# Performance work log

Measured on AMD Instinct MI355X. Metric: run time of the kernel, lower is better.

The kernel has to match this reference:

```python
import jax, jax.numpy as jnp
import numpy as np

DIM = 1024
HEAD_DIM = 64
NUM_HEADS = DIM // HEAD_DIM
SCALE = HEAD_DIM ** -0.5


def setup_inputs() -> dict:
    key = jax.random.key(0)
    ks = jax.random.split(key, 12)
    b, n = 4, 2048
    std = DIM ** -0.5
    inp = {
        'words': jax.random.normal(ks[0], (b, n, DIM), jnp.float32),
        'position': jax.random.normal(ks[1], (b, n, DIM), jnp.float32),
        'conscious': jax.random.normal(ks[2], (b, n, DIM), jnp.float32),
        # projection weights stored as [in, out] (torch Linear W^T)
        'w_wq': jax.random.normal(ks[3], (DIM, DIM), jnp.float32) * std,
        'w_wk': jax.random.normal(ks[4], (DIM, DIM), jnp.float32) * std,
        'w_wv': jax.random.normal(ks[5], (DIM, DIM), jnp.float32) * std,
        'w_pq': jax.random.normal(ks[6], (DIM, DIM), jnp.float32) * std,
        'w_pk': jax.random.normal(ks[7], (DIM, DIM), jnp.float32) * std,
        'w_cq': jax.random.normal(ks[8], (DIM, DIM), jnp.float32) * std,
        'w_ck': jax.random.normal(ks[9], (DIM, DIM), jnp.float32) * std,
        'w_out': jax.random.normal(ks[10], (DIM, DIM), jnp.float32) * std,
        'b_out': jax.random.normal(ks[11], (DIM,), jnp.float32) * 0.01,
    }
    return inp


def _heads(x):
    b, n, _ = x.shape
    return x.reshape(b, n, NUM_HEADS, HEAD_DIM).transpose(0, 2, 1, 3)  # b h n d


def reference(words, position, conscious, w_wq, w_wk, w_wv, w_pq, w_pk, w_cq, w_ck, w_out, b_out):
    # fused multi-source q/k: sum of three projections per source
    q = _heads(words @ w_wq + position @ w_pq + conscious @ w_cq)
    k = _heads(words @ w_wk + position @ w_pk + conscious @ w_ck)
    v = _heads(words @ w_wv)
    sim = jnp.einsum('bhid,bhjd->bhij', q, k) * SCALE
    attn = jax.nn.softmax(sim, axis=-1)
    out = jnp.einsum('bhij,bhjd->bhid', attn, v)
    b, h, n, d = out.shape
    out = out.transpose(0, 2, 1, 3).reshape(b, n, h * d)
    return out @ w_out + b_out
```

## Files before the change

kernel.cpp:

```cpp
#include <hip/hip_runtime.h>
#include <hip/hip_bf16.h>

typedef __bf16 bf16_t;
typedef __attribute__((ext_vector_type(8))) __bf16 bf16x8;
typedef __attribute__((ext_vector_type(4))) float f32x4;
typedef __attribute__((ext_vector_type(16))) float f32x16;

__device__ __forceinline__ void gld_lds16(const void* g, void* l) {
  __builtin_amdgcn_global_load_lds((const __attribute__((address_space(1))) void*)g,
                                   (__attribute__((address_space(3))) void*)l, 16, 0, 0);
}

__global__ __launch_bounds__(256) void cast_concat(
    const float* __restrict__ w, const float* __restrict__ p,
    const float* __restrict__ c, bf16_t* __restrict__ X)
{
  unsigned idx = blockIdx.x * 256u + threadIdx.x;
  unsigned src = idx >> 21;
  unsigned rem = idx & ((1u << 21) - 1);
  unsigned row = rem >> 8;
  unsigned k4  = (rem & 255u) * 4u;
  const float* s = (src == 0) ? w : (src == 1) ? p : c;
  f32x4 v = *(const f32x4*)(s + (size_t)row * 1024 + k4);
  ushort4 u;
  u.x = __builtin_bit_cast(unsigned short, (bf16_t)v[0]);
  u.y = __builtin_bit_cast(unsigned short, (bf16_t)v[1]);
  u.z = __builtin_bit_cast(unsigned short, (bf16_t)v[2]);
  u.w = __builtin_bit_cast(unsigned short, (bf16_t)v[3]);
  *(ushort4*)(X + (size_t)row * 3072 + src * 1024 + k4) = u;
}

__global__ __launch_bounds__(256) void transpose_all(
    const float* __restrict__ w_wq, const float* __restrict__ w_pq,
    const float* __restrict__ w_cq, const float* __restrict__ w_wk,
    const float* __restrict__ w_pk, const float* __restrict__ w_ck,
    const float* __restrict__ w_wv, const float* __restrict__ w_out,
    bf16_t* __restrict__ Wqkt, bf16_t* __restrict__ Wvt, bf16_t* __restrict__ Wot)
{
  __shared__ float t[32][33];
  const int z = blockIdx.z;
  const float* src; bf16_t* dst; int dstride, koff, roff;
  switch (z) {
    case 0: src = w_wq;  dst = Wqkt; dstride = 3072; koff = 0;    roff = 0;    break;
    case 1: src = w_pq;  dst = Wqkt; dstride = 3072; koff = 1024; roff = 0;    break;
    case 2: src = w_cq;  dst = Wqkt; dstride = 3072; koff = 2048; roff = 0;    break;
    case 3: src = w_wk;  dst = Wqkt; dstride = 3072; koff = 0;    roff = 1024; break;
    case 4: src = w_pk;  dst = Wqkt; dstride = 3072; koff = 1024; roff = 1024; break;
    case 5: src = w_ck;  dst = Wqkt; dstride = 3072; koff = 2048; roff = 1024; break;
    case 6: src = w_wv;  dst = Wvt;  dstride = 1024; koff = 0;    roff = 0;    break;
    default: src = w_out; dst = Wot; dstride = 1024; koff = 0;    roff = 0;    break;
  }
  int bx = blockIdx.x, by = blockIdx.y;
  int x = bx * 32 + threadIdx.x;
  int y0 = by * 32;
  for (int i = threadIdx.y; i < 32; i += 8)
    t[i][threadIdx.x] = src[(size_t)(y0 + i) * 1024 + x];
  __syncthreads();
  int n0 = bx * 32;
  for (int i = threadIdx.y; i < 32; i += 8)
    dst[(size_t)(n0 + i + roff) * dstride + koff + y0 + threadIdx.x] =
        (bf16_t)t[threadIdx.x][i];
}

__global__ __launch_bounds__(512, 2) void gemm256_qk(
    const bf16_t* __restrict__ A, int lda,
    const bf16_t* __restrict__ Bt, int K,
    bf16_t* __restrict__ Qo, bf16_t* __restrict__ Ko, float scale, int nbx)
{
  __shared__ bf16_t As[2][256 * 64];
  __shared__ bf16_t Bs[2][256 * 64];

  const int tid = threadIdx.x;
  const int wave = tid >> 6, lane = tid & 63;
  const int wm = wave >> 2, wn = wave & 3;
  const int lrow = lane & 15, lch = lane >> 4;

  const int nwg = gridDim.x, cpx = nwg >> 3;
  const int id  = blockIdx.x;
  const int swz = (id & 7) * cpx + (id >> 3);
  const int mb = swz / nbx, nb = swz % nbx;
  const int m0 = mb * 256, n0 = nb * 256;

  const int srow = tid >> 3, spp = tid & 7;

  auto STAGE = [&](int buf, int k0) {
#pragma unroll
    for (int i = 0; i < 4; ++i) {
      int r = i * 64 + srow;
      int gsw = (spp ^ (r & 7)) * 8;
      gld_lds16(A + (size_t)(m0 + r) * lda + k0 + gsw, &As[buf][r * 64 + spp * 8]);
    }
#pragma unroll
    for (int i = 0; i < 4; ++i) {
      int r = i * 64 + srow;
      int gsw = (spp ^ (r & 7)) * 8;
      gld_lds16(Bt + (size_t)(n0 + r) * K + k0 + gsw, &Bs[buf][r * 64 + spp * 8]);
    }
  };

  const int NT = K >> 6;
  STAGE(0, 0);
  STAGE(1, 64);

  f32x4 acc[8][4] = {};

  for (int kt = 0; kt < NT; ++kt) {
    const int cur = kt & 1;
    if (kt < NT - 1) {
      asm volatile("s_waitcnt vmcnt(8)" ::: "memory");
    } else {
      asm volatile("s_waitcnt vmcnt(0)" ::: "memory");
    }
    asm volatile("s_barrier" ::: "memory");

#pragma unroll
    for (int ks = 0; ks < 2; ++ks) {
      bf16x8 af[8], bfr[4];
#pragma unroll
      for (int m = 0; m < 8; ++m) {
        int r = wm * 128 + m * 16 + lrow;
        af[m] = *(const bf16x8*)&As[cur][r * 64 + (((ks * 4 + lch) ^ (r & 7)) * 8)];
      }
#pragma unroll
      for (int n = 0; n < 4; ++n) {
        int r = wn * 64 + n * 16 + lrow;
        bfr[n] = *(const bf16x8*)&Bs[cur][r * 64 + (((ks * 4 + lch) ^ (r & 7)) * 8)];
      }
      __builtin_amdgcn_s_setprio(1);
#pragma unroll
      for (int m = 0; m < 8; ++m)
#pragma unroll
        for (int n = 0; n < 4; ++n)
          acc[m][n] = __builtin_amdgcn_mfma_f32_16x16x32_bf16(af[m], bfr[n], acc[m][n], 0, 0, 0);
      __builtin_amdgcn_s_setprio(0);
    }

    asm volatile("s_waitcnt lgkmcnt(0)" ::: "memory");
    asm volatile("s_barrier" ::: "memory");
    if (kt + 2 < NT) STAGE(cur, (kt + 2) * 64);
  }

  const int g = lane >> 4, cl = lane & 15;
#pragma unroll
  for (int m = 0; m < 8; ++m) {
    int m_base = m0 + wm * 128 + m * 16 + g * 4;
    int bb = m_base >> 11, nn = m_base & 2047;
#pragma unroll
    for (int n = 0; n < 4; ++n) {
      int col = n0 + wn * 64 + n * 16 + cl;
      bf16_t* dst = (col < 1024) ? Qo : Ko;
      int cc2 = col & 1023;
      float sc = (col < 1024) ? scale : 1.0f;
      int h = cc2 >> 6, d = cc2 & 63;
      size_t base = ((size_t)(bb * 16 + h) * 2048 + nn) * 64 + d;
#pragma unroll
      for (int r = 0; r < 4; ++r)
        dst[base + (size_t)r * 64] = (bf16_t)(acc[m][n][r] * sc);
    }
  }
}

template<int EPI>
__global__ __launch_bounds__(512, 2) void gemm128x256(
    const bf16_t* __restrict__ A, int lda,
    const bf16_t* __restrict__ Bt, int K,
    void* __restrict__ Cout, const float* __restrict__ bias)
{
  __shared__ bf16_t As[2][128 * 64];
  __shared__ bf16_t Bs[2][256 * 64];

  const int tid = threadIdx.x;
  const int wave = tid >> 6, lane = tid & 63;
  const int wm = wave >> 2, wn = wave & 3;
  const int lrow = lane & 15, lch = lane >> 4;

  const int nwg = gridDim.x, cpx = nwg >> 3;
  const int id  = blockIdx.x;
  const int swz = (id & 7) * cpx + (id >> 3);
  const int mb = swz >> 2, nb = swz & 3;
  const int m0 = mb * 128, n0 = nb * 256;

  const int srow = tid >> 3, spp = tid & 7;

  auto STAGE = [&](int buf, int k0) {
#pragma unroll
    for (int i = 0; i < 2; ++i) {
      int r = i * 64 + srow;
      int gsw = (spp ^ (r & 7)) * 8;
      gld_lds16(A + (size_t)(m0 + r) * lda + k0 + gsw, &As[buf][r * 64 + spp * 8]);
    }
#pragma unroll
    for (int i = 0; i < 4; ++i) {
      int r = i * 64 + srow;
      int gsw = (spp ^ (r & 7)) * 8;
      gld_lds16(Bt + (size_t)(n0 + r) * K + k0 + gsw, &Bs[buf][r * 64 + spp * 8]);
    }
  };

  const int NT = K >> 6;
  STAGE(0, 0);
  STAGE(1, 64);

  f32x4 acc[4][4] = {};

  for (int kt = 0; kt < NT; ++kt) {
    const int cur = kt & 1;
    if (kt < NT - 1) {
      asm volatile("s_waitcnt vmcnt(6)" ::: "memory");
    } else {
      asm volatile("s_waitcnt vmcnt(0)" ::: "memory");
    }
    asm volatile("s_barrier" ::: "memory");

#pragma unroll
    for (int ks = 0; ks < 2; ++ks) {
      bf16x8 af[4], bfr[4];
#pragma unroll
      for (int m = 0; m < 4; ++m) {
        int r = wm * 64 + m * 16 + lrow;
        af[m] = *(const bf16x8*)&As[cur][r * 64 + (((ks * 4 + lch) ^ (r & 7)) * 8)];
      }
#pragma unroll
      for (int n = 0; n < 4; ++n) {
        int r = wn * 64 + n * 16 + lrow;
        bfr[n] = *(const bf16x8*)&Bs[cur][r * 64 + (((ks * 4 + lch) ^ (r & 7)) * 8)];
      }
      __builtin_amdgcn_s_setprio(1);
#pragma unroll
      for (int m = 0; m < 4; ++m)
#pragma unroll
        for (int n = 0; n < 4; ++n)
          acc[m][n] = __builtin_amdgcn_mfma_f32_16x16x32_bf16(af[m], bfr[n], acc[m][n], 0, 0, 0);
      __builtin_amdgcn_s_setprio(0);
    }

    asm volatile("s_waitcnt lgkmcnt(0)" ::: "memory");
    asm volatile("s_barrier" ::: "memory");
    if (kt + 2 < NT) STAGE(cur, (kt + 2) * 64);
  }

  const int g = lane >> 4, cl = lane & 15;
  if (EPI == 1) {
    bf16_t* Vo = (bf16_t*)Cout;
#pragma unroll
    for (int m = 0; m < 4; ++m) {
      int m_base = m0 + wm * 64 + m * 16 + g * 4;
      int bb = m_base >> 11, nn = m_base & 2047;
#pragma unroll
      for (int n = 0; n < 4; ++n) {
        int col = n0 + wn * 64 + n * 16 + cl;
        int h = col >> 6, d = col & 63;
        ushort4 u;
        u.x = __builtin_bit_cast(unsigned short, (bf16_t)acc[m][n][0]);
        u.y = __builtin_bit_cast(unsigned short, (bf16_t)acc[m][n][1]);
        u.z = __builtin_bit_cast(unsigned short, (bf16_t)acc[m][n][2]);
        u.w = __builtin_bit_cast(unsigned short, (bf16_t)acc[m][n][3]);
        *(ushort4*)(Vo + ((size_t)(bb * 16 + h) * 64 + d) * 2048 + nn) = u;
      }
    }
  } else {
    float* Co = (float*)Cout;
#pragma unroll
    for (int m = 0; m < 4; ++m) {
      int m_base = m0 + wm * 64 + m * 16 + g * 4;
#pragma unroll
      for (int n = 0; n < 4; ++n) {
        int col = n0 + wn * 64 + n * 16 + cl;
        float bv = bias[col];
#pragma unroll
        for (int r = 0; r < 4; ++r)
          Co[(size_t)(m_base + r) * 1024 + col] = acc[m][n][r] + bv;
      }
    }
  }
}

__global__ __launch_bounds__(512, 2) void attn_kernel(
    const bf16_t* __restrict__ Q, const bf16_t* __restrict__ Kb,
    const bf16_t* __restrict__ Vt, bf16_t* __restrict__ O)
{
  __shared__ bf16_t Ks[2][64 * 64];
  __shared__ bf16_t Vs[2][64 * 64];

  const int fid = blockIdx.x;
  const int swz = (fid & 7) * 64 + (fid >> 3);
  const int bh = swz >> 3, qt = swz & 7;
  const int bb = bh >> 4, h = bh & 15;

  const int tid = threadIdx.x, wave = tid >> 6, lane = tid & 63;
  const int lq = lane & 31;
  const int lh = lane >> 5;

  const bf16_t* Qb    = Q  + ((size_t)bh * 2048 + qt * 256) * 64;
  const bf16_t* Kbase = Kb + (size_t)bh * 2048 * 64;
  const bf16_t* Vbase = Vt + (size_t)bh * 64 * 2048;

  const int srow = tid >> 3, spp = tid & 7;
  const int sgr = (spp ^ (srow & 7)) * 8;

  auto STAGE_K = [&](int buf, int tile) {
    gld_lds16(Kbase + (size_t)(tile * 64 + srow) * 64 + sgr, &Ks[buf][tid * 8]);
  };
  auto STAGE_V = [&](int buf, int tile) {
    gld_lds16(Vbase + (size_t)srow * 2048 + tile * 64 + sgr, &Vs[buf][tid * 8]);
  };

  STAGE_K(0, 0); STAGE_V(0, 0); STAGE_K(1, 1);

  bf16x8 qf[4];
#pragma unroll
  for (int kf = 0; kf < 4; ++kf)
    qf[kf] = *(const bf16x8*)(Qb + (size_t)(wave * 32 + lq) * 64 + kf * 16 + lh * 8);

  f32x16 acc[2] = {};
  float m_run = -1.0e30f, l_run = 0.f;
  bf16x8 pb[4];

  auto QKT = [&](int tile, f32x16 (&st)[2]) {
    const int kb = tile & 1;
#pragma unroll
    for (int nb2 = 0; nb2 < 2; ++nb2) {
      int r = nb2 * 32 + lq;
      f32x16 z = {};
#pragma unroll
      for (int kf = 0; kf < 4; ++kf) {
        bf16x8 ka = *(const bf16x8*)&Ks[kb][r * 64 + (((kf * 2 + lh) ^ (r & 7)) * 8)];
        z = __builtin_amdgcn_mfma_f32_32x32x16_bf16(ka, qf[kf], z, 0, 0, 0);
      }
      st[nb2] = z;
    }
  };

  auto PV = [&](int tile) {
    const int vb = tile & 1;
#pragma unroll
    for (int ks = 0; ks < 4; ++ks)
#pragma unroll
      for (int db = 0; db < 2; ++db) {
        int r = db * 32 + lq;
        bf16x8 va = *(const bf16x8*)&Vs[vb][r * 64 + (((ks * 2 + lh) ^ (r & 7)) * 8)];
        acc[db] = __builtin_amdgcn_mfma_f32_32x32x16_bf16(va, pb[ks], acc[db], 0, 0, 0);
      }
  };

  auto SOFTMAX = [&](f32x16 (&st)[2]) {
    float tmax = fmaxf(st[0][0], st[0][1]);
#pragma unroll
    for (int nb2 = 0; nb2 < 2; ++nb2)
#pragma unroll
      for (int rg = (nb2 ? 0 : 2); rg < 16; rg += 2)
        tmax = fmaxf(fmaxf(tmax, st[nb2][rg]), st[nb2][rg + 1]);
    tmax = fmaxf(tmax, __shfl_xor(tmax, 32));

    if (!__all(tmax <= m_run + 8.0f)) {
      float mnew = fmaxf(m_run, tmax);
      float corr = __builtin_amdgcn_exp2f(m_run - mnew);
      m_run = mnew;
      l_run *= corr;
#pragma unroll
      for (int db = 0; db < 2; ++db)
#pragma unroll
        for (int rg = 0; rg < 16; ++rg)
          acc[db][rg] *= corr;
    }

    float sm = 0.f;
#pragma unroll
    for (int nb2 = 0; nb2 < 2; ++nb2)
#pragma unroll
      for (int rg = 0; rg < 16; ++rg) {
        float p = __builtin_amdgcn_exp2f(st[nb2][rg] - m_run);
        st[nb2][rg] = p;
        sm += p;
      }
    sm += __shfl_xor(sm, 32);
    l_run += sm;

#pragma unroll
    for (int ks = 0; ks < 4; ++ks) {
      const int nb2 = ks >> 1;
      const int R = (ks & 1) * 8;
      unsigned x0, x1, y0, y1;
      asm("v_cvt_pk_bf16_f32 %0, %1, %2" : "=v"(x0) : "v"(st[nb2][R + 0]), "v"(st[nb2][R + 1]));
      asm("v_cvt_pk_bf16_f32 %0, %1, %2" : "=v"(x1) : "v"(st[nb2][R + 2]), "v"(st[nb2][R + 3]));
      asm("v_cvt_pk_bf16_f32 %0, %1, %2" : "=v"(y0) : "v"(st[nb2][R + 4]), "v"(st[nb2][R + 5]));
      asm("v_cvt_pk_bf16_f32 %0, %1, %2" : "=v"(y1) : "v"(st[nb2][R + 6]), "v"(st[nb2][R + 7]));
      asm volatile("v_permlane32_swap_b32 %0, %1" : "+v"(x0), "+v"(y0));
      asm volatile("v_permlane32_swap_b32 %0, %1" : "+v"(x1), "+v"(y1));
      int4 pw;
      pw.x = (int)x0; pw.y = (int)x1; pw.z = (int)y0; pw.w = (int)y1;
      pb[ks] = __builtin_bit_cast(bf16x8, pw);
    }
  };

  asm volatile("s_waitcnt vmcnt(0)" ::: "memory");
  __builtin_amdgcn_s_barrier();
  asm volatile("" ::: "memory");
  {
    f32x16 st[2];
    QKT(0, st);
    SOFTMAX(st);
  }
  asm volatile("s_waitcnt lgkmcnt(0)" ::: "memory");
  __builtin_amdgcn_s_barrier();
  asm volatile("" ::: "memory");

  for (int t = 0; t < 32; ++t) {
    if (t < 30)       { STAGE_V((t + 1) & 1, t + 1); STAGE_K(t & 1, t + 2); }
    else if (t == 30) { STAGE_V(1, 31); }
    if (t < 30)       asm volatile("s_waitcnt vmcnt(2)" ::: "memory");
    else if (t == 30) asm volatile("s_waitcnt vmcnt(1)" ::: "memory");
    else              asm volatile("s_waitcnt vmcnt(0)" ::: "memory");
    __builtin_amdgcn_s_barrier();
    asm volatile("" ::: "memory");

    f32x16 st[2];
    __builtin_amdgcn_s_setprio(1);
    if (t < 31) QKT(t + 1, st);
    PV(t);
    __builtin_amdgcn_s_setprio(0);
    if (t < 31) SOFTMAX(st);

    asm volatile("s_waitcnt lgkmcnt(0)" ::: "memory");
    __builtin_amdgcn_s_barrier();
    asm volatile("" ::: "memory");
  }

  float inv = 1.0f / l_run;
  int nn = qt * 256 + wave * 32 + lq;
  size_t obase = ((size_t)bb * 2048 + nn) * 1024 + h * 64;
#pragma unroll
  for (int db = 0; db < 2; ++db)
#pragma unroll
    for (int rr = 0; rr < 4; ++rr) {
      ushort4 u;
      u.x = __builtin_bit_cast(unsigned short, (bf16_t)(acc[db][rr * 4 + 0] * inv));
      u.y = __builtin_bit_cast(unsigned short, (bf16_t)(acc[db][rr * 4 + 1] * inv));
      u.z = __builtin_bit_cast(unsigned short, (bf16_t)(acc[db][rr * 4 + 2] * inv));
      u.w = __builtin_bit_cast(unsigned short, (bf16_t)(acc[db][rr * 4 + 3] * inv));
      *(ushort4*)(O + obase + db * 32 + rr * 8 + lh * 4) = u;
    }
}

extern "C" void kernel_launch(void* const* d_in, const int* in_sizes, int n_in,
                              void* d_out, int out_size, void* d_ws, size_t ws_size,
                              hipStream_t stream) {
  const float* words     = (const float*)d_in[0];
  const float* position  = (const float*)d_in[1];
  const float* conscious = (const float*)d_in[2];
  const float* w_wq  = (const float*)d_in[3];
  const float* w_wk  = (const float*)d_in[4];
  const float* w_wv  = (const float*)d_in[5];
  const float* w_pq  = (const float*)d_in[6];
  const float* w_pk  = (const float*)d_in[7];
  const float* w_cq  = (const float*)d_in[8];
  const float* w_ck  = (const float*)d_in[9];
  const float* w_out = (const float*)d_in[10];
  const float* b_out = (const float*)d_in[11];

  char* ws = (char*)d_ws;
  bf16_t* Xcat = (bf16_t*)(ws);
  bf16_t* Wqkt = (bf16_t*)(ws + 50331648);
  bf16_t* Wvt  = (bf16_t*)(ws + 62914560);
  bf16_t* Wot  = (bf16_t*)(ws + 65011712);
  bf16_t* Qb   = (bf16_t*)(ws + 67108864);
  bf16_t* Kbf  = (bf16_t*)(ws + 83886080);
  bf16_t* Vtb  = (bf16_t*)(ws + 100663296);
  bf16_t* Ob   = (bf16_t*)(ws + 117440512);

  cast_concat<<<24576, 256, 0, stream>>>(words, position, conscious, Xcat);

  transpose_all<<<dim3(32, 32, 8), dim3(32, 8), 0, stream>>>(
      w_wq, w_pq, w_cq, w_wk, w_pk, w_ck, w_wv, w_out, Wqkt, Wvt, Wot);

  gemm256_qk<<<256, 512, 0, stream>>>(Xcat, 3072, Wqkt, 3072, Qb, Kbf,
                                      0.125f * 1.44269504f, 8);
  gemm128x256<1><<<256, 512, 0, stream>>>(Xcat, 3072, Wvt, 1024, Vtb, nullptr);

  attn_kernel<<<512, 512, 0, stream>>>(Qb, Kbf, Vtb, Ob);

  gemm128x256<2><<<256, 512, 0, stream>>>(Ob, 1024, Wot, 1024, (float*)d_out, b_out);
}
```

Baseline: 288.6 us.

## Process two 32-row query blocks per wave in attention, halving block threads

The attention kernel now uses 256 threads (4 waves) per block, and each wave handles 64 query rows as two 32-row sub-blocks. Each K/V fragment read from LDS feeds two MFMAs, which halves LDS read traffic per MFMA. Staging is split so each thread issues two async loads per tile, and the vmcnt waits are adjusted to match. The cost is roughly double the accumulator and score registers per wave, fewer waves per block to hide latency, and two softmax passes per wave.

```diff
diff --git a/kernel.cpp b/kernel.cpp
--- a/kernel.cpp
+++ b/kernel.cpp
@@ -275,7 +275,7 @@
   }
 }
 
-__global__ __launch_bounds__(512, 2) void attn_kernel(
+__global__ __launch_bounds__(256, 2) void attn_kernel(
     const bf16_t* __restrict__ Q, const bf16_t* __restrict__ Kb,
     const bf16_t* __restrict__ Vt, bf16_t* __restrict__ O)
 {
@@ -296,42 +296,54 @@
   const bf16_t* Vbase = Vt + (size_t)bh * 64 * 2048;
 
   const int srow = tid >> 3, spp = tid & 7;
-  const int sgr = (spp ^ (srow & 7)) * 8;
 
   auto STAGE_K = [&](int buf, int tile) {
-    gld_lds16(Kbase + (size_t)(tile * 64 + srow) * 64 + sgr, &Ks[buf][tid * 8]);
+#pragma unroll
+    for (int i = 0; i < 2; ++i) {
+      int r = i * 32 + srow;
+      int sg = (spp ^ (r & 7)) * 8;
+      gld_lds16(Kbase + (size_t)(tile * 64 + r) * 64 + sg, &Ks[buf][i * 2048 + tid * 8]);
+    }
   };
   auto STAGE_V = [&](int buf, int tile) {
-    gld_lds16(Vbase + (size_t)srow * 2048 + tile * 64 + sgr, &Vs[buf][tid * 8]);
+#pragma unroll
+    for (int i = 0; i < 2; ++i) {
+      int r = i * 32 + srow;
+      int sg = (spp ^ (r & 7)) * 8;
+      gld_lds16(Vbase + (size_t)r * 2048 + tile * 64 + sg, &Vs[buf][i * 2048 + tid * 8]);
+    }
   };
 
   STAGE_K(0, 0); STAGE_V(0, 0); STAGE_K(1, 1);
 
-  bf16x8 qf[4];
-#pragma unroll
-  for (int kf = 0; kf < 4; ++kf)
-    qf[kf] = *(const bf16x8*)(Qb + (size_t)(wave * 32 + lq) * 64 + kf * 16 + lh * 8);
-
-  f32x16 acc[2] = {};
-  float m_run = -1.0e30f, l_run = 0.f;
-  bf16x8 pb[4];
-
-  auto QKT = [&](int tile, f32x16 (&st)[2]) {
+  bf16x8 qf0[4], qf1[4];
+#pragma unroll
+  for (int kf = 0; kf < 4; ++kf) {
+    qf0[kf] = *(const bf16x8*)(Qb + (size_t)(wave * 64 + lq) * 64 + kf * 16 + lh * 8);
+    qf1[kf] = *(const bf16x8*)(Qb + (size_t)(wave * 64 + 32 + lq) * 64 + kf * 16 + lh * 8);
+  }
+
+  f32x16 acc0[2] = {}, acc1[2] = {};
+  float m0r = -1.0e30f, l0r = 0.f, m1r = -1.0e30f, l1r = 0.f;
+  bf16x8 pb0[4], pb1[4];
+
+  auto QKT2 = [&](int tile, f32x16 (&s0)[2], f32x16 (&s1)[2]) {
     const int kb = tile & 1;
 #pragma unroll
     for (int nb2 = 0; nb2 < 2; ++nb2) {
       int r = nb2 * 32 + lq;
-      f32x16 z = {};
+      f32x16 z0 = {}, z1 = {};
 #pragma unroll
       for (int kf = 0; kf < 4; ++kf) {
         bf16x8 ka = *(const bf16x8*)&Ks[kb][r * 64 + (((kf * 2 + lh) ^ (r & 7)) * 8)];
-        z = __builtin_amdgcn_mfma_f32_32x32x16_bf16(ka, qf[kf], z, 0, 0, 0);
-      }
-      st[nb2] = z;
-    }
-  };
-
-  auto PV = [&](int tile) {
+        z0 = __builtin_amdgcn_mfma_f32_32x32x16_bf16(ka, qf0[kf], z0, 0, 0, 0);
+        z1 = __builtin_amdgcn_mfma_f32_32x32x16_bf16(ka, qf1[kf], z1, 0, 0, 0);
+      }
+      s0[nb2] = z0; s1[nb2] = z1;
+    }
+  };
+
+  auto PV2 = [&](int tile) {
     const int vb = tile & 1;
 #pragma unroll
     for (int ks = 0; ks < 4; ++ks)
@@ -339,11 +351,13 @@
       for (int db = 0; db < 2; ++db) {
         int r = db * 32 + lq;
         bf16x8 va = *(const bf16x8*)&Vs[vb][r * 64 + (((ks * 2 + lh) ^ (r & 7)) * 8)];
-        acc[db] = __builtin_amdgcn_mfma_f32_32x32x16_bf16(va, pb[ks], acc[db], 0, 0, 0);
-      }
-  };
-
-  auto SOFTMAX = [&](f32x16 (&st)[2]) {
+        acc0[db] = __builtin_amdgcn_mfma_f32_32x32x16_bf16(va, pb0[ks], acc0[db], 0, 0, 0);
+        acc1[db] = __builtin_amdgcn_mfma_f32_32x32x16_bf16(va, pb1[ks], acc1[db], 0, 0, 0);
+      }
+  };
+
+  auto SOFTMAX = [&](f32x16 (&st)[2], float& mr, float& lr,
+                     f32x16 (&ac)[2], bf16x8 (&po)[4]) {
     float tmax = fmaxf(st[0][0], st[0][1]);
 #pragma unroll
     for (int nb2 = 0; nb2 < 2; ++nb2)
@@ -352,16 +366,16 @@
         tmax = fmaxf(fmaxf(tmax, st[nb2][rg]), st[nb2][rg + 1]);
     tmax = fmaxf(tmax, __shfl_xor(tmax, 32));
 
-    if (!__all(tmax <= m_run + 8.0f)) {
-      float mnew = fmaxf(m_run, tmax);
-      float corr = __builtin_amdgcn_exp2f(m_run - mnew);
-      m_run = mnew;
-      l_run *= corr;
+    if (!__all(tmax <= mr + 8.0f)) {
+      float mnew = fmaxf(mr, tmax);
+      float corr = __builtin_amdgcn_exp2f(mr - mnew);
+      mr = mnew;
+      lr *= corr;
 #pragma unroll
       for (int db = 0; db < 2; ++db)
 #pragma unroll
         for (int rg = 0; rg < 16; ++rg)
-          acc[db][rg] *= corr;
+          ac[db][rg] *= corr;
     }
 
     float sm = 0.f;
@@ -369,12 +383,12 @@
     for (int nb2 = 0; nb2 < 2; ++nb2)
 #pragma unroll
       for (int rg = 0; rg < 16; ++rg) {
-        float p = __builtin_amdgcn_exp2f(st[nb2][rg] - m_run);
+        float p = __builtin_amdgcn_exp2f(st[nb2][rg] - mr);
         st[nb2][rg] = p;
         sm += p;
       }
     sm += __shfl_xor(sm, 32);
-    l_run += sm;
+    lr += sm;
 
 #pragma unroll
     for (int ks = 0; ks < 4; ++ks) {
@@ -389,7 +403,7 @@
       asm volatile("v_permlane32_swap_b32 %0, %1" : "+v"(x1), "+v"(y1));
       int4 pw;
       pw.x = (int)x0; pw.y = (int)x1; pw.z = (int)y0; pw.w = (int)y1;
-      pb[ks] = __builtin_bit_cast(bf16x8, pw);
+      po[ks] = __builtin_bit_cast(bf16x8, pw);
     }
   };
 
@@ -397,9 +411,10 @@
   __builtin_amdgcn_s_barrier();
   asm volatile("" ::: "memory");
   {
-    f32x16 st[2];
-    QKT(0, st);
-    SOFTMAX(st);
+    f32x16 s0[2], s1[2];
+    QKT2(0, s0, s1);
+    SOFTMAX(s0, m0r, l0r, acc0, pb0);
+    SOFTMAX(s1, m1r, l1r, acc1, pb1);
   }
   asm volatile("s_waitcnt lgkmcnt(0)" ::: "memory");
   __builtin_amdgcn_s_barrier();
@@ -408,38 +423,46 @@
   for (int t = 0; t < 32; ++t) {
     if (t < 30)       { STAGE_V((t + 1) & 1, t + 1); STAGE_K(t & 1, t + 2); }
     else if (t == 30) { STAGE_V(1, 31); }
-    if (t < 30)       asm volatile("s_waitcnt vmcnt(2)" ::: "memory");
-    else if (t == 30) asm volatile("s_waitcnt vmcnt(1)" ::: "memory");
+    if (t < 30)       asm volatile("s_waitcnt vmcnt(4)" ::: "memory");
+    else if (t == 30) asm volatile("s_waitcnt vmcnt(2)" ::: "memory");
     else              asm volatile("s_waitcnt vmcnt(0)" ::: "memory");
     __builtin_amdgcn_s_barrier();
     asm volatile("" ::: "memory");
 
-    f32x16 st[2];
+    f32x16 s0[2], s1[2];
     __builtin_amdgcn_s_setprio(1);
-    if (t < 31) QKT(t + 1, st);
-    PV(t);
+    if (t < 31) QKT2(t + 1, s0, s1);
+    PV2(t);
     __builtin_amdgcn_s_setprio(0);
-    if (t < 31) SOFTMAX(st);
+    if (t < 31) {
+      SOFTMAX(s0, m0r, l0r, acc0, pb0);
+      SOFTMAX(s1, m1r, l1r, acc1, pb1);
+    }
 
     asm volatile("s_waitcnt lgkmcnt(0)" ::: "memory");
     __builtin_amdgcn_s_barrier();
     asm volatile("" ::: "memory");
   }
 
-  float inv = 1.0f / l_run;
-  int nn = qt * 256 + wave * 32 + lq;
-  size_t obase = ((size_t)bb * 2048 + nn) * 1024 + h * 64;
-#pragma unroll
-  for (int db = 0; db < 2; ++db)
-#pragma unroll
-    for (int rr = 0; rr < 4; ++rr) {
-      ushort4 u;
-      u.x = __builtin_bit_cast(unsigned short, (bf16_t)(acc[db][rr * 4 + 0] * inv));
-      u.y = __builtin_bit_cast(unsigned short, (bf16_t)(acc[db][rr * 4 + 1] * inv));
-      u.z = __builtin_bit_cast(unsigned short, (bf16_t)(acc[db][rr * 4 + 2] * inv));
-      u.w = __builtin_bit_cast(unsigned short, (bf16_t)(acc[db][rr * 4 + 3] * inv));
-      *(ushort4*)(O + obase + db * 32 + rr * 8 + lh * 4) = u;
-    }
+  float inv0 = 1.0f / l0r, inv1 = 1.0f / l1r;
+#pragma unroll
+  for (int qb = 0; qb < 2; ++qb) {
+    float inv = qb ? inv1 : inv0;
+    int nn = qt * 256 + wave * 64 + qb * 32 + lq;
+    size_t obase = ((size_t)bb * 2048 + nn) * 1024 + h * 64;
+#pragma unroll
+    for (int db = 0; db < 2; ++db)
+#pragma unroll
+      for (int rr = 0; rr < 4; ++rr) {
+        f32x16& a = qb ? acc1[db] : acc0[db];
+        ushort4 u;
+        u.x = __builtin_bit_cast(unsigned short, (bf16_t)(a[rr * 4 + 0] * inv));
+        u.y = __builtin_bit_cast(unsigned short, (bf16_t)(a[rr * 4 + 1] * inv));
+        u.z = __builtin_bit_cast(unsigned short, (bf16_t)(a[rr * 4 + 2] * inv));
+        u.w = __builtin_bit_cast(unsigned short, (bf16_t)(a[rr * 4 + 3] * inv));
+        *(ushort4*)(O + obase + db * 32 + rr * 8 + lh * 4) = u;
+      }
+  }
 }
 
 extern "C" void kernel_launch(void* const* d_in, const int* in_sizes, int n_in,
@@ -477,7 +500,7 @@
                                       0.125f * 1.44269504f, 8);
   gemm128x256<1><<<256, 512, 0, stream>>>(Xcat, 3072, Wvt, 1024, Vtb, nullptr);
 
-  attn_kernel<<<512, 512, 0, stream>>>(Qb, Kbf, Vtb, Ob);
+  attn_kernel<<<512, 256, 0, stream>>>(Qb, Kbf, Vtb, Ob);
 
   gemm128x256<2><<<256, 512, 0, stream>>>(Ob, 1024, Wot, 1024, (float*)d_out, b_out);
 }
```

After: 281.7 us. -2.4%, faster.
